# Kernel optimization log

Measured on AMD Instinct MI355X. Metric: run time of the kernel, lower is better.

Reference implementation:

```python
import jax, jax.numpy as jnp
import numpy as np

B, N = 16, 16384
K = 16        # num_keypoints
LATENT = 128
CAGE = 8
BN_EPS = 1e-5


def setup_inputs():
    key = jax.random.key(0)
    ks = jax.random.split(key, 40)
    def rn(i, shape, s=1.0):
        return jax.random.normal(ks[i], shape, dtype=jnp.float32) * s
    inp = {
        "source_points": rn(0, (B, N, 3)),
        "target_points": rn(1, (B, N, 3)),
        "enc_w1": rn(2, (64, 3), 0.3), "enc_b1": rn(3, (64,), 0.1),
        "bn1_gamma": 1.0 + rn(4, (64,), 0.1), "bn1_beta": rn(5, (64,), 0.1),
        "bn1_mean": rn(6, (64,), 0.1), "bn1_var": 0.5 + jax.random.uniform(ks[7], (64,), dtype=jnp.float32),
        "enc_w2": rn(8, (128, 64), 0.1), "enc_b2": rn(9, (128,), 0.1),
        "bn2_gamma": 1.0 + rn(10, (128,), 0.1), "bn2_beta": rn(11, (128,), 0.1),
        "bn2_mean": rn(12, (128,), 0.1), "bn2_var": 0.5 + jax.random.uniform(ks[13], (128,), dtype=jnp.float32),
        "enc_w3": rn(14, (LATENT, 128), 0.1), "enc_b3": rn(15, (LATENT,), 0.1),
        "bn3_gamma": 1.0 + rn(16, (LATENT,), 0.1), "bn3_beta": rn(17, (LATENT,), 0.1),
        "bn3_mean": rn(18, (LATENT,), 0.1), "bn3_var": 0.5 + jax.random.uniform(ks[19], (LATENT,), dtype=jnp.float32),
        "kp_w1": rn(20, (128, LATENT), 0.1), "kp_b1": rn(21, (128,), 0.1),
        "kp_w2": rn(22, (K * 3, 128), 0.1), "kp_b2": rn(23, (K * 3,), 0.1),
        "cg_w1": rn(24, (128, K * 3), 0.1), "cg_b1": rn(25, (128,), 0.1),
        "cg_w2": rn(26, (CAGE ** 3 * 3, 128), 0.05), "cg_b2": rn(27, (CAGE ** 3 * 3,), 0.01),
    }
    return inp


def _bn(x, g, b, m, v):
    # inference-mode BatchNorm1d over channel (last) dim
    return (x - m) * jax.lax.rsqrt(v + BN_EPS) * g + b


def _encode(pts, w1, b1, g1, be1, m1, v1, w2, b2, g2, be2, m2, v2, w3, b3, g3, be3, m3, v3):
    # pointwise 1x1 convs == per-point linear layers; pts: (B, N, 3)
    h = jax.nn.relu(_bn(jnp.einsum('bnc,oc->bno', pts, w1) + b1, g1, be1, m1, v1))
    h = jax.nn.relu(_bn(jnp.einsum('bnc,oc->bno', h, w2) + b2, g2, be2, m2, v2))
    h = jax.nn.relu(_bn(jnp.einsum('bnc,oc->bno', h, w3) + b3, g3, be3, m3, v3))
    return h.max(axis=1)  # global max-pool -> (B, LATENT)


def _fps_one(pts, kps):
    # pts: (N,3), kps: (K,3). Same math as the torch loop: iterative farthest-point
    # selection; recomputing cdist to selected[:i] each step == incremental min-dist.
    # squared distances preserve argmax/min of euclidean distances.
    d0 = jnp.sum((pts[:, None, :] - kps[None, :, :]) ** 2, -1).min(axis=1)
    sel0 = pts[jnp.argmax(d0)]
    mind = jnp.sum((pts - sel0) ** 2, -1)
    def step(mind, _):
        sel = pts[jnp.argmax(mind)]
        return jnp.minimum(mind, jnp.sum((pts - sel) ** 2, -1)), sel
    _, sels = jax.lax.scan(step, mind, None, length=K - 1)
    return jnp.concatenate([sel0[None], sels], axis=0)  # (K, 3)


def _fps(points, keypoints):
    return jax.vmap(_fps_one)(points, keypoints)


def _cage_deform(pts, disp):
    # pts: (B,N,3), disp: (B,C,C,C,3). Batched trilinear interpolation on the cage.
    C = CAGE
    lin = jnp.linspace(0.0, 1.0, C)
    grid = jnp.stack(jnp.meshgrid(lin, lin, lin, indexing='ij'), axis=-1)
    cage = grid[None] + disp
    cf = cage.reshape(cage.shape[0], C * C * C, 3)
    pmin = pts.min(axis=1, keepdims=True)
    pmax = pts.max(axis=1, keepdims=True)
    t = (pts - pmin) / (pmax - pmin + 1e-6) * (C - 1)
    idx = jnp.clip(t.astype(jnp.int32), 0, C - 2)   # trunc == floor (t >= 0)
    w = t - idx.astype(t.dtype)
    u, v, z = idx[..., 0], idx[..., 1], idx[..., 2]
    wx, wy, wz = w[..., 0:1], w[..., 1:2], w[..., 2:3]
    def corner(du, dv, dz):
        flat = (u + du) * C * C + (v + dv) * C + (z + dz)      # (B,N)
        flat = jnp.broadcast_to(flat[..., None], flat.shape + (3,))
        return jnp.take_along_axis(cf, flat, axis=1)            # (B,N,3)
    d = ((1 - wx) * (1 - wy) * (1 - wz) * corner(0, 0, 0)
         + wx * (1 - wy) * (1 - wz) * corner(1, 0, 0)
         + (1 - wx) * wy * (1 - wz) * corner(0, 1, 0)
         + wx * wy * (1 - wz) * corner(1, 1, 0)
         + (1 - wx) * (1 - wy) * wz * corner(0, 0, 1)
         + wx * (1 - wy) * wz * corner(1, 0, 1)
         + (1 - wx) * wy * wz * corner(0, 1, 1)
         + wx * wy * wz * corner(1, 1, 1))
    return pts + d


def reference(source_points, target_points, enc_w1, enc_b1, bn1_gamma, bn1_beta, bn1_mean, bn1_var, enc_w2, enc_b2, bn2_gamma, bn2_beta, bn2_mean, bn2_var, enc_w3, enc_b3, bn3_gamma, bn3_beta, bn3_mean, bn3_var, kp_w1, kp_b1, kp_w2, kp_b2, cg_w1, cg_b1, cg_w2, cg_b2):
    enc = lambda p: _encode(p, enc_w1, enc_b1, bn1_gamma, bn1_beta, bn1_mean, bn1_var,
                            enc_w2, enc_b2, bn2_gamma, bn2_beta, bn2_mean, bn2_var,
                            enc_w3, enc_b3, bn3_gamma, bn3_beta, bn3_mean, bn3_var)
    src_lat = enc(source_points)
    tgt_lat = enc(target_points)
    kp = lambda lat: (jax.nn.relu(lat @ kp_w1.T + kp_b1) @ kp_w2.T + kp_b2).reshape(-1, K, 3)
    src_kp = _fps(source_points, kp(src_lat))
    tgt_kp = _fps(target_points, kp(tgt_lat))
    diff = (tgt_kp - src_kp).reshape(-1, K * 3)
    disp = (jax.nn.relu(diff @ cg_w1.T + cg_b1) @ cg_w2.T + cg_b2).reshape(-1, CAGE, CAGE, CAGE, 3)
    deformed = _cage_deform(source_points, disp)
    return (deformed, src_kp, tgt_kp)
```

## Files before the change

### kernel.cpp

```cpp
#include <hip/hip_runtime.h>

#define B_ 16
#define N_ 16384
#define K_ 16

enum : int {
  WS_LAT  = 0,
  WS_SEL  = 5632,
  WS_PMIN = 7168,
  WS_PMAX = 7216,
  WS_CF   = 7264,
  WS_W1F  = 31840,
  WS_B1F  = 32032,
  WS_WB2H = 32096,
  WS_WB2L = 36192,
  WS_B2F  = 40288,
  WS_WB3H = 40416,
  WS_B3F  = 56800,
  WS_WB3L = 56928,
  WS_END  = 73312
};

enum : int { OUT_DEF=0, OUT_SRCKP=786432, OUT_TGTKP=787200 };

typedef _Float16 f16x8 __attribute__((ext_vector_type(8)));
typedef _Float16 f16x2 __attribute__((ext_vector_type(2)));
typedef float    f32x4 __attribute__((ext_vector_type(4)));

__device__ __forceinline__ float dist2rn(float px,float py,float pz,float sx,float sy,float sz){
  float dx=__fsub_rn(px,sx), dy=__fsub_rn(py,sy), dz=__fsub_rn(pz,sz);
  return __fadd_rn(__fadd_rn(__fmul_rn(dx,dx),__fmul_rn(dy,dy)),__fmul_rn(dz,dz));
}

struct EncW {
  const float *w1,*b1,*g1,*be1,*m1,*v1;
  const float *w2,*b2,*g2,*be2,*m2,*v2;
  const float *w3,*b3,*g3,*be3,*m3,*v3;
};

__device__ __forceinline__ float bn_scale(const float* g, const float* v, int ch){
  return g[ch] * (1.0f / sqrtf(v[ch] + 1e-5f));
}

__global__ void prep_kernel(EncW a, float* ws){
  const int stride = gridDim.x*blockDim.x;
  const int tid = blockIdx.x*blockDim.x + threadIdx.x;
  for (int i=tid;i<4096;i+=stride)
    ws[WS_LAT+i] = 0.0f;
  for (int i=tid;i<192;i+=stride){
    int o=i/3;
    ws[WS_W1F+i] = a.w1[i] * bn_scale(a.g1,a.v1,o);
  }
  for (int i=tid;i<64;i+=stride){
    float s = bn_scale(a.g1,a.v1,i);
    ws[WS_B1F+i] = (a.b1[i] - a.m1[i])*s + a.be1[i];
  }
  for (int i=tid;i<8192;i+=stride){
    int j = i & 7, frag = i >> 3;
    int l = frag & 63, nk = frag >> 6;
    int kt = nk & 1, nt = nk >> 1;
    int c = kt*32 + ((l>>4)<<3) + j;
    int o = nt*16 + (l&15);
    float v = a.w2[o*64+c] * bn_scale(a.g2,a.v2,o);
    _Float16 h = (_Float16)v;
    ((_Float16*)(ws+WS_WB2H))[i] = h;
    ((_Float16*)(ws+WS_WB2L))[i] = (_Float16)(v - (float)h);
  }
  for (int i=tid;i<128;i+=stride){
    float s = bn_scale(a.g2,a.v2,i);
    ws[WS_B2F+i] = (a.b2[i] - a.m2[i])*s + a.be2[i];
  }
  for (int i=tid;i<32768;i+=stride){
    int j = i & 7, frag = i >> 3;
    int l = frag & 63, nk = frag >> 6;
    int kt = nk & 3, nt = nk >> 2;
    int c = kt*32 + ((l>>4)<<3) + j;
    int o = nt*16 + (l&15);
    float v = a.w3[o*128+c] * bn_scale(a.g3,a.v3,o);
    _Float16 h = (_Float16)v;
    ((_Float16*)(ws+WS_WB3H))[i] = h;
    ((_Float16*)(ws+WS_WB3L))[i] = (_Float16)(v - (float)h);
  }
  for (int i=tid;i<128;i+=stride){
    float s = bn_scale(a.g3,a.v3,i);
    ws[WS_B3F+i] = (a.b3[i] - a.m3[i])*s + a.be3[i];
  }
}

__global__ __launch_bounds__(512, 4) void encode_kernel(const float* __restrict__ src,
                                                        const float* __restrict__ tgt,
                                                        const float* __restrict__ ws,
                                                        float* __restrict__ lat){
  const int cloud = blockIdx.y;
  const int tile  = blockIdx.x;
  const int t = threadIdx.x;
  const int lane = t & 63;
  const int wv = __builtin_amdgcn_readfirstlane(t >> 6);
  const int wm = wv >> 2;
  const int wn = wv & 3;
  const int lr = lane & 15;
  const int lg = lane >> 4;

  __shared__ alignas(16) _Float16 A[32768];
  _Float16* AH1 = A;
  _Float16* AL1 = A + 8192;
  _Float16* AH2 = A;
  _Float16* AL2 = A + 16384;

  const float* base = ((cloud < B_) ? (src + (size_t)cloud*N_*3)
                                    : (tgt + (size_t)(cloud-B_)*N_*3))
                      + (size_t)tile*128*3;

  {
    const int pt = t >> 2, q = t & 3;
    const float x = base[pt*3+0], y = base[pt*3+1], z = base[pt*3+2];
    const float* w1 = ws + WS_W1F;
    const float* b1 = ws + WS_B1F;
    const int swz = (pt & 7) << 3;
    #pragma unroll
    for (int cc = 0; cc < 16; cc += 2){
      const int o = q*16 + cc;
      float v0 = fmaf(w1[o*3+2], z, fmaf(w1[o*3+1], y, w1[o*3+0]*x)) + b1[o];
      float v1 = fmaf(w1[o*3+5], z, fmaf(w1[o*3+4], y, w1[o*3+3]*x)) + b1[o+1];
      v0 = fmaxf(v0, 0.0f); v1 = fmaxf(v1, 0.0f);
      f16x2 h, l;
      h[0] = (_Float16)v0;              h[1] = (_Float16)v1;
      l[0] = (_Float16)(v0 - (float)h[0]); l[1] = (_Float16)(v1 - (float)h[1]);
      const int idx = (pt*64 + o) ^ swz;
      *(f16x2*)&AH1[idx] = h;
      *(f16x2*)&AL1[idx] = l;
    }
  }
  __syncthreads();

  f32x4 acc2[4][2];
  #pragma unroll
  for (int m=0;m<4;m++){
    #pragma unroll
    for (int n=0;n<2;n++) acc2[m][n] = (f32x4){0.f,0.f,0.f,0.f};
  }
  {
    const _Float16* wb2h = (const _Float16*)(ws + WS_WB2H);
    const _Float16* wb2l = (const _Float16*)(ws + WS_WB2L);
    const int swz = (lr & 7) << 3;
    #pragma unroll
    for (int kt=0; kt<2; kt++){
      f16x8 bh[2], bl[2];
      #pragma unroll
      for (int n=0;n<2;n++){
        const int fi = (((wn*2+n)*2 + kt)*64 + lane)*8;
        bh[n] = *(const f16x8*)(wb2h + fi);
        bl[n] = *(const f16x8*)(wb2l + fi);
      }
      #pragma unroll
      for (int m=0;m<4;m++){
        const int row = wm*64 + m*16 + lr;
        const int idx = (row*64 + kt*32 + lg*8) ^ swz;
        const f16x8 ah = *(const f16x8*)&AH1[idx];
        const f16x8 al = *(const f16x8*)&AL1[idx];
        #pragma unroll
        for (int n=0;n<2;n++){
          acc2[m][n] = __builtin_amdgcn_mfma_f32_16x16x32_f16(ah, bh[n], acc2[m][n], 0,0,0);
          acc2[m][n] = __builtin_amdgcn_mfma_f32_16x16x32_f16(ah, bl[n], acc2[m][n], 0,0,0);
          acc2[m][n] = __builtin_amdgcn_mfma_f32_16x16x32_f16(al, bh[n], acc2[m][n], 0,0,0);
        }
      }
    }
  }
  __syncthreads();

  {
    const float* b2 = ws + WS_B2F;
    #pragma unroll
    for (int n=0;n<2;n++){
      const int ch = wn*32 + n*16 + lr;
      const float b = b2[ch];
      #pragma unroll
      for (int m=0;m<4;m++){
        #pragma unroll
        for (int r=0;r<4;r++){
          const int row = wm*64 + m*16 + lg*4 + r;
          const float v = fmaxf(acc2[m][n][r] + b, 0.0f);
          const _Float16 hi = (_Float16)v;
          const _Float16 lo = (_Float16)(v - (float)hi);
          const int idx = (row*128 + ch) ^ ((row & 7) << 3);
          AH2[idx] = hi;
          AL2[idx] = lo;
        }
      }
    }
  }
  __syncthreads();

  f32x4 acc3[4][2];
  #pragma unroll
  for (int m=0;m<4;m++){
    #pragma unroll
    for (int n=0;n<2;n++) acc3[m][n] = (f32x4){0.f,0.f,0.f,0.f};
  }
  {
    const _Float16* wb3h = (const _Float16*)(ws + WS_WB3H);
    const _Float16* wb3l = (const _Float16*)(ws + WS_WB3L);
    const int swz = (lr & 7) << 3;
    #pragma unroll
    for (int kt=0; kt<4; kt++){
      f16x8 bh[2], bl[2];
      #pragma unroll
      for (int n=0;n<2;n++){
        const int fi = (((wn*2+n)*4 + kt)*64 + lane)*8;
        bh[n] = *(const f16x8*)(wb3h + fi);
        bl[n] = *(const f16x8*)(wb3l + fi);
      }
      #pragma unroll
      for (int m=0;m<4;m++){
        const int row = wm*64 + m*16 + lr;
        const int idx = (row*128 + kt*32 + lg*8) ^ swz;
        const f16x8 ah = *(const f16x8*)&AH2[idx];
        const f16x8 al = *(const f16x8*)&AL2[idx];
        #pragma unroll
        for (int n=0;n<2;n++){
          acc3[m][n] = __builtin_amdgcn_mfma_f32_16x16x32_f16(ah, bh[n], acc3[m][n], 0,0,0);
          acc3[m][n] = __builtin_amdgcn_mfma_f32_16x16x32_f16(ah, bl[n], acc3[m][n], 0,0,0);
          acc3[m][n] = __builtin_amdgcn_mfma_f32_16x16x32_f16(al, bh[n], acc3[m][n], 0,0,0);
        }
      }
    }
  }

  {
    const float* b3 = ws + WS_B3F;
    #pragma unroll
    for (int n=0;n<2;n++){
      const int ch = wn*32 + n*16 + lr;
      const float b = b3[ch];
      float x = 0.0f;
      #pragma unroll
      for (int m=0;m<4;m++){
        #pragma unroll
        for (int r=0;r<4;r++)
          x = fmaxf(x, acc3[m][n][r] + b);
      }
      x = fmaxf(x, __shfl_xor(x, 16, 64));
      x = fmaxf(x, __shfl_xor(x, 32, 64));
      if (lane < 16)
        atomicMax((unsigned*)(lat + cloud*128 + ch), __float_as_uint(x));
    }
  }
}

__global__ __launch_bounds__(512) void fps_kernel(const float* __restrict__ src,
                                                  const float* __restrict__ tgt,
                                                  const float* __restrict__ kw1,
                                                  const float* __restrict__ kb1,
                                                  const float* __restrict__ kw2,
                                                  const float* __restrict__ kb2,
                                                  float* ws, float* out){
  const int cloud = blockIdx.x; const int t = threadIdx.x;
  const float* base = (cloud < B_) ? (src + (size_t)cloud*N_*3)
                                   : (tgt + (size_t)(cloud-B_)*N_*3);
  __shared__ float kpl[48];
  __shared__ float h[128];
  __shared__ float rv[512]; __shared__ int ri[512];
  __shared__ float sel[3];

  float px[32], py[32], pz[32];
  #pragma unroll
  for (int k=0;k<32;k++){
    int n = t + k*512;
    px[k]=base[n*3]; py[k]=base[n*3+1]; pz[k]=base[n*3+2];
  }

  const float* lat = ws + WS_LAT + cloud*128;
  if (t < 128){
    float acc = kb1[t];
    const float* w = kw1 + t*128;
    for (int c=0;c<128;c++) acc = fmaf(lat[c], w[c], acc);
    h[t] = fmaxf(acc, 0.0f);
  }
  __syncthreads();
  if (t < 48){
    float acc = kb2[t];
    const float* w = kw2 + t*128;
    for (int c=0;c<128;c++) acc = fmaf(h[c], w[c], acc);
    kpl[t] = acc;
  }
  __syncthreads();

  float mnx=3.4e38f,mny=3.4e38f,mnz=3.4e38f, mxx=-3.4e38f,mxy=-3.4e38f,mxz=-3.4e38f;
  float bv = -1.0f; int bi = 0;
  #pragma unroll 2
  for (int k=0;k<32;k++){
    int n = t + k*512;
    if (cloud < B_){
      mnx=fminf(mnx,px[k]); mny=fminf(mny,py[k]); mnz=fminf(mnz,pz[k]);
      mxx=fmaxf(mxx,px[k]); mxy=fmaxf(mxy,py[k]); mxz=fmaxf(mxz,pz[k]);
    }
    float dmin = 3.4028235e38f;
    #pragma unroll
    for (int j=0;j<K_;j++)
      dmin = fminf(dmin, dist2rn(px[k],py[k],pz[k], kpl[j*3],kpl[j*3+1],kpl[j*3+2]));
    if (dmin > bv){ bv = dmin; bi = n; }
  }

  rv[t]=bv; ri[t]=bi;
  __syncthreads();
  if (t < 64){
    float v = rv[t]; int i = ri[t];
    #pragma unroll
    for (int e=1;e<8;e++){
      float v2=rv[t+64*e]; int i2=ri[t+64*e];
      if (v2 > v || (v2 == v && i2 < i)){ v=v2; i=i2; }
    }
    #pragma unroll
    for (int m=1;m<64;m<<=1){
      float v2=__shfl_xor(v,m,64); int i2=__shfl_xor(i,m,64);
      if (v2 > v || (v2 == v && i2 < i)){ v=v2; i=i2; }
    }
    if (t==0){
      sel[0]=base[i*3]; sel[1]=base[i*3+1]; sel[2]=base[i*3+2];
      float* sw = ws + WS_SEL + cloud*48;
      sw[0]=sel[0]; sw[1]=sel[1]; sw[2]=sel[2];
      size_t o = (cloud<B_) ? (size_t)(OUT_SRCKP + cloud*48) : (size_t)(OUT_TGTKP + (cloud-B_)*48);
      out[o]=sel[0]; out[o+1]=sel[1]; out[o+2]=sel[2];
    }
  }
  __syncthreads();

  if (cloud < B_){
    float vals[6] = {mnx,mny,mnz,mxx,mxy,mxz};
    for (int c=0;c<6;c++){
      rv[t]=vals[c];
      __syncthreads();
      if (t < 64){
        float v = rv[t];
        #pragma unroll
        for (int e=1;e<8;e++){
          float v2 = rv[t+64*e];
          v = (c<3) ? fminf(v,v2) : fmaxf(v,v2);
        }
        #pragma unroll
        for (int m=1;m<64;m<<=1){
          float v2=__shfl_xor(v,m,64);
          v = (c<3) ? fminf(v,v2) : fmaxf(v,v2);
        }
        if (t==0){
          if (c<3) ws[WS_PMIN + cloud*3 + c] = v;
          else     ws[WS_PMAX + cloud*3 + (c-3)] = v;
        }
      }
      __syncthreads();
    }
  }

  float s0=sel[0], s1=sel[1], s2=sel[2];

  float mind[32];
  bv = -1.0f; bi = 0;
  #pragma unroll
  for (int k=0;k<32;k++){
    int n = t + k*512;
    float d = dist2rn(px[k],py[k],pz[k], s0,s1,s2);
    mind[k]=d;
    if (d > bv){ bv=d; bi=n; }
  }

  for (int it=1; it<K_; it++){
    rv[t]=bv; ri[t]=bi;
    __syncthreads();
    if (t < 64){
      float v = rv[t]; int i = ri[t];
      #pragma unroll
      for (int e=1;e<8;e++){
        float v2=rv[t+64*e]; int i2=ri[t+64*e];
        if (v2 > v || (v2 == v && i2 < i)){ v=v2; i=i2; }
      }
      #pragma unroll
      for (int m=1;m<64;m<<=1){
        float v2=__shfl_xor(v,m,64); int i2=__shfl_xor(i,m,64);
        if (v2 > v || (v2 == v && i2 < i)){ v=v2; i=i2; }
      }
      if (t==0){
        sel[0]=base[i*3]; sel[1]=base[i*3+1]; sel[2]=base[i*3+2];
        float* sw = ws + WS_SEL + cloud*48 + it*3;
        sw[0]=sel[0]; sw[1]=sel[1]; sw[2]=sel[2];
        size_t o = (cloud<B_) ? (size_t)(OUT_SRCKP + cloud*48 + it*3)
                              : (size_t)(OUT_TGTKP + (cloud-B_)*48 + it*3);
        out[o]=sel[0]; out[o+1]=sel[1]; out[o+2]=sel[2];
      }
    }
    __syncthreads();
    s0=sel[0]; s1=sel[1]; s2=sel[2];
    if (it < K_-1){
      bv=-1.0f; bi=0;
      #pragma unroll
      for (int k=0;k<32;k++){
        int n = t + k*512;
        float d = dist2rn(px[k],py[k],pz[k], s0,s1,s2);
        float m = fminf(mind[k], d);
        mind[k]=m;
        if (m > bv){ bv=m; bi=n; }
      }
    }
  }
}

__global__ void cage_mlp_kernel(const float* __restrict__ ws,
                                const float* __restrict__ cw1, const float* __restrict__ cb1,
                                const float* __restrict__ cw2, const float* __restrict__ cb2,
                                float* __restrict__ wsm){
  const int b = blockIdx.x >> 2, part = blockIdx.x & 3;
  const int t = threadIdx.x;
  __shared__ float diff[48]; __shared__ float h[128];
  if (t<48) diff[t] = __fsub_rn(ws[WS_SEL + (B_+b)*48 + t], ws[WS_SEL + b*48 + t]);
  __syncthreads();
  if (t<128){
    const float* w = cw1 + t*48;
    float acc = cb1[t];
    for (int j=0;j<48;j++) acc = fmaf(diff[j], w[j], acc);
    h[t] = fmaxf(acc, 0.0f);
  }
  __syncthreads();
  for (int o = part*384 + t; o < part*384 + 384; o += 256){
    const float* w = cw2 + o*128;
    float acc = cb2[o];
    for (int c=0;c<128;c++) acc = fmaf(h[c], w[c], acc);
    int flat = o/3, coord = o - flat*3;
    int u = flat>>6, v=(flat>>3)&7, z=flat&7;
    int g = (coord==0)?u:((coord==1)?v:z);
    float gv = (g==7)?1.0f:(float)g*(1.0f/7.0f);
    wsm[WS_CF + b*1536 + o] = gv + acc;
  }
}

__global__ __launch_bounds__(256) void deform_kernel(const float* __restrict__ src,
                                                     const float* __restrict__ ws,
                                                     float* __restrict__ out){
  const int b = blockIdx.y;
  const int n = blockIdx.x*256 + threadIdx.x;
  __shared__ float cf[1536];
  for (int i=threadIdx.x;i<1536;i+=256) cf[i] = ws[WS_CF + b*1536 + i];
  __syncthreads();

  const float* p = src + ((size_t)b*N_ + n)*3;
  float pt[3]; int id[3]; float w[3];
  #pragma unroll
  for (int c=0;c<3;c++){
    float pv = p[c];
    float mn = ws[WS_PMIN+b*3+c], mxv = ws[WS_PMAX+b*3+c];
    float denom = __fadd_rn(__fsub_rn(mxv, mn), 1e-6f);
    float tc = __fmul_rn(__fdiv_rn(__fsub_rn(pv, mn), denom), 7.0f);
    int ic = (int)tc; ic = min(max(ic,0),6);
    pt[c]=pv; id[c]=ic; w[c]=__fsub_rn(tc, (float)ic);
  }
  const int flat = (id[0]<<6) + (id[1]<<3) + id[2];
  const float* c000 = cf + flat*3;
  const float wx=w[0], wy=w[1], wz=w[2];
  const float ux=__fsub_rn(1.0f,wx), uy=__fsub_rn(1.0f,wy), uz=__fsub_rn(1.0f,wz);
  const float w000=__fmul_rn(__fmul_rn(ux,uy),uz);
  const float w100=__fmul_rn(__fmul_rn(wx,uy),uz);
  const float w010=__fmul_rn(__fmul_rn(ux,wy),uz);
  const float w110=__fmul_rn(__fmul_rn(wx,wy),uz);
  const float w001=__fmul_rn(__fmul_rn(ux,uy),wz);
  const float w101=__fmul_rn(__fmul_rn(wx,uy),wz);
  const float w011=__fmul_rn(__fmul_rn(ux,wy),wz);
  const float w111=__fmul_rn(__fmul_rn(wx,wy),wz);
  #pragma unroll
  for (int c=0;c<3;c++){
    float d = __fmul_rn(w000, c000[c]);
    d = __fadd_rn(d, __fmul_rn(w100, c000[192+c]));
    d = __fadd_rn(d, __fmul_rn(w010, c000[24+c]));
    d = __fadd_rn(d, __fmul_rn(w110, c000[216+c]));
    d = __fadd_rn(d, __fmul_rn(w001, c000[3+c]));
    d = __fadd_rn(d, __fmul_rn(w101, c000[195+c]));
    d = __fadd_rn(d, __fmul_rn(w011, c000[27+c]));
    d = __fadd_rn(d, __fmul_rn(w111, c000[219+c]));
    out[((size_t)b*N_+n)*3 + c] = __fadd_rn(pt[c], d);
  }
}

extern "C" void kernel_launch(void* const* d_in, const int* in_sizes, int n_in,
                              void* d_out, int out_size, void* d_ws, size_t ws_size,
                              hipStream_t stream){
  const float* src = (const float*)d_in[0];
  const float* tgt = (const float*)d_in[1];
  float* ws = (float*)d_ws;
  float* out = (float*)d_out;

  EncW ew;
  ew.w1 =(const float*)d_in[2];  ew.b1 =(const float*)d_in[3];
  ew.g1 =(const float*)d_in[4];  ew.be1=(const float*)d_in[5];
  ew.m1 =(const float*)d_in[6];  ew.v1 =(const float*)d_in[7];
  ew.w2 =(const float*)d_in[8];  ew.b2 =(const float*)d_in[9];
  ew.g2 =(const float*)d_in[10]; ew.be2=(const float*)d_in[11];
  ew.m2 =(const float*)d_in[12]; ew.v2 =(const float*)d_in[13];
  ew.w3 =(const float*)d_in[14]; ew.b3 =(const float*)d_in[15];
  ew.g3 =(const float*)d_in[16]; ew.be3=(const float*)d_in[17];
  ew.m3 =(const float*)d_in[18]; ew.v3 =(const float*)d_in[19];

  prep_kernel<<<128, 256, 0, stream>>>(ew, ws);
  encode_kernel<<<dim3(128,32), 512, 0, stream>>>(src, tgt, ws, ws + WS_LAT);
  fps_kernel<<<32, 512, 0, stream>>>(src, tgt,
      (const float*)d_in[20], (const float*)d_in[21],
      (const float*)d_in[22], (const float*)d_in[23], ws, out);
  cage_mlp_kernel<<<64, 256, 0, stream>>>(ws,
      (const float*)d_in[24], (const float*)d_in[25],
      (const float*)d_in[26], (const float*)d_in[27], ws);
  deform_kernel<<<dim3(64,16), 256, 0, stream>>>(src, ws, out);
}
```

Before: 302.6 us.

## Restructure FPS kernel with 1024 threads, single-barrier rounds, and separate minmax kernel

Moves the per-cloud bounding-box min/max out of the FPS kernel into a new minmax_kernel that writes order-preserving encoded floats through atomics. The FPS kernel now runs 1024 threads per cloud, and each thread loads 16 contiguous points with float4 reads. Each round does a wave-level shuffle argmax and carries the winner's coordinates, so a single barrier and double-buffered shared slots replace the two-barrier shared reduction and the global reload of the selected point. The intent is to cut per-iteration latency in the serial 16-round FPS loop, at the cost of an extra kernel launch and atomic traffic.

```diff
diff --git a/kernel.cpp b/kernel.cpp
--- a/kernel.cpp
+++ b/kernel.cpp
@@ -32,6 +32,14 @@
   return __fadd_rn(__fadd_rn(__fmul_rn(dx,dx),__fmul_rn(dy,dy)),__fmul_rn(dz,dz));
 }
 
+__device__ __forceinline__ unsigned enc_ord(float x){
+  unsigned u = __float_as_uint(x);
+  return (u & 0x80000000u) ? ~u : (u | 0x80000000u);
+}
+__device__ __forceinline__ float dec_ord(unsigned e){
+  return __uint_as_float((e & 0x80000000u) ? (e & 0x7fffffffu) : ~e);
+}
+
 struct EncW {
   const float *w1,*b1,*g1,*be1,*m1,*v1;
   const float *w2,*b2,*g2,*be2,*m2,*v2;
@@ -47,6 +55,10 @@
   const int tid = blockIdx.x*blockDim.x + threadIdx.x;
   for (int i=tid;i<4096;i+=stride)
     ws[WS_LAT+i] = 0.0f;
+  for (int i=tid;i<48;i+=stride){
+    ((unsigned*)ws)[WS_PMIN+i] = 0xFFFFFFFFu;
+    ((unsigned*)ws)[WS_PMAX+i] = 0u;
+  }
   for (int i=tid;i<192;i+=stride){
     int o=i/3;
     ws[WS_W1F+i] = a.w1[i] * bn_scale(a.g1,a.v1,o);
@@ -84,6 +96,38 @@
   for (int i=tid;i<128;i+=stride){
     float s = bn_scale(a.g3,a.v3,i);
     ws[WS_B3F+i] = (a.b3[i] - a.m3[i])*s + a.be3[i];
+  }
+}
+
+__global__ __launch_bounds__(256) void minmax_kernel(const float* __restrict__ src,
+                                                     float* __restrict__ ws){
+  const int b = blockIdx.y, c = blockIdx.x, t = threadIdx.x;
+  const float4* b4 = (const float4*)(src + (size_t)b*N_*3 + (size_t)c*2048*3 + (size_t)t*24);
+  float a[24];
+  #pragma unroll
+  for (int q=0;q<6;q++){ float4 v=b4[q]; a[q*4]=v.x; a[q*4+1]=v.y; a[q*4+2]=v.z; a[q*4+3]=v.w; }
+  float mn[3]={3.4e38f,3.4e38f,3.4e38f}, mx[3]={-3.4e38f,-3.4e38f,-3.4e38f};
+  #pragma unroll
+  for (int k=0;k<8;k++){
+    mn[0]=fminf(mn[0],a[k*3  ]); mx[0]=fmaxf(mx[0],a[k*3  ]);
+    mn[1]=fminf(mn[1],a[k*3+1]); mx[1]=fmaxf(mx[1],a[k*3+1]);
+    mn[2]=fminf(mn[2],a[k*3+2]); mx[2]=fmaxf(mx[2],a[k*3+2]);
+  }
+  #pragma unroll
+  for (int m=1;m<64;m<<=1){
+    #pragma unroll
+    for (int cc=0;cc<3;cc++){
+      mn[cc]=fminf(mn[cc],__shfl_xor(mn[cc],m,64));
+      mx[cc]=fmaxf(mx[cc],__shfl_xor(mx[cc],m,64));
+    }
+  }
+  if ((t&63)==0){
+    unsigned* wsu = (unsigned*)ws;
+    #pragma unroll
+    for (int cc=0;cc<3;cc++){
+      atomicMin(&wsu[WS_PMIN + b*3 + cc], enc_ord(mn[cc]));
+      atomicMax(&wsu[WS_PMAX + b*3 + cc], enc_ord(mx[cc]));
+    }
   }
 }
 
@@ -248,26 +292,61 @@
   }
 }
 
-__global__ __launch_bounds__(512) void fps_kernel(const float* __restrict__ src,
-                                                  const float* __restrict__ tgt,
-                                                  const float* __restrict__ kw1,
-                                                  const float* __restrict__ kb1,
-                                                  const float* __restrict__ kw2,
-                                                  const float* __restrict__ kb2,
-                                                  float* ws, float* out){
+__device__ __forceinline__ void fps_round(int r, int t, int wv,
+                                          float bv, int bi, float bx, float by, float bz,
+                                          float (*cv)[16], int (*ci)[16],
+                                          float (*cx)[16], float (*cy)[16], float (*cz)[16],
+                                          float* ws, float* out, int cloud,
+                                          float& s0, float& s1, float& s2){
+  float v = bv; int i = bi;
+  #pragma unroll
+  for (int m=1;m<64;m<<=1){
+    float v2=__shfl_xor(v,m,64); int i2=__shfl_xor(i,m,64);
+    if (v2 > v || (v2 == v && i2 < i)){ v=v2; i=i2; }
+  }
+  const int p = r & 1;
+  if ((i >> 4) == t){ cv[p][wv]=v; ci[p][wv]=i; cx[p][wv]=bx; cy[p][wv]=by; cz[p][wv]=bz; }
+  __syncthreads();
+  float wvv = cv[p][0]; int wi = ci[p][0]; int ws_slot = 0;
+  #pragma unroll
+  for (int e=1;e<16;e++){
+    float v2=cv[p][e]; int i2=ci[p][e];
+    if (v2 > wvv || (v2 == wvv && i2 < wi)){ wvv=v2; wi=i2; ws_slot=e; }
+  }
+  s0 = cx[p][ws_slot]; s1 = cy[p][ws_slot]; s2 = cz[p][ws_slot];
+  if (t == 0){
+    float* sw = ws + WS_SEL + cloud*48 + r*3;
+    sw[0]=s0; sw[1]=s1; sw[2]=s2;
+    size_t o = (cloud<B_) ? (size_t)(OUT_SRCKP + cloud*48 + r*3)
+                          : (size_t)(OUT_TGTKP + (cloud-B_)*48 + r*3);
+    out[o]=s0; out[o+1]=s1; out[o+2]=s2;
+  }
+}
+
+__global__ __launch_bounds__(1024) void fps_kernel(const float* __restrict__ src,
+                                                   const float* __restrict__ tgt,
+                                                   const float* __restrict__ kw1,
+                                                   const float* __restrict__ kb1,
+                                                   const float* __restrict__ kw2,
+                                                   const float* __restrict__ kb2,
+                                                   float* ws, float* out){
   const int cloud = blockIdx.x; const int t = threadIdx.x;
+  const int wv = t >> 6;
   const float* base = (cloud < B_) ? (src + (size_t)cloud*N_*3)
                                    : (tgt + (size_t)(cloud-B_)*N_*3);
   __shared__ float kpl[48];
   __shared__ float h[128];
-  __shared__ float rv[512]; __shared__ int ri[512];
-  __shared__ float sel[3];
-
-  float px[32], py[32], pz[32];
-  #pragma unroll
-  for (int k=0;k<32;k++){
-    int n = t + k*512;
-    px[k]=base[n*3]; py[k]=base[n*3+1]; pz[k]=base[n*3+2];
+  __shared__ float cv[2][16]; __shared__ int ci[2][16];
+  __shared__ float cx[2][16]; __shared__ float cy[2][16]; __shared__ float cz[2][16];
+
+  float px[16], py[16], pz[16];
+  {
+    const float4* b4 = (const float4*)(base + (size_t)t*48);
+    float a[48];
+    #pragma unroll
+    for (int q=0;q<12;q++){ float4 v=b4[q]; a[q*4]=v.x; a[q*4+1]=v.y; a[q*4+2]=v.z; a[q*4+3]=v.w; }
+    #pragma unroll
+    for (int k=0;k<16;k++){ px[k]=a[k*3]; py[k]=a[k*3+1]; pz[k]=a[k*3+2]; }
   }
 
   const float* lat = ws + WS_LAT + cloud*128;
@@ -286,121 +365,43 @@
   }
   __syncthreads();
 
-  float mnx=3.4e38f,mny=3.4e38f,mnz=3.4e38f, mxx=-3.4e38f,mxy=-3.4e38f,mxz=-3.4e38f;
-  float bv = -1.0f; int bi = 0;
-  #pragma unroll 2
-  for (int k=0;k<32;k++){
-    int n = t + k*512;
-    if (cloud < B_){
-      mnx=fminf(mnx,px[k]); mny=fminf(mny,py[k]); mnz=fminf(mnz,pz[k]);
-      mxx=fmaxf(mxx,px[k]); mxy=fmaxf(mxy,py[k]); mxz=fmaxf(mxz,pz[k]);
-    }
-    float dmin = 3.4028235e38f;
-    #pragma unroll
-    for (int j=0;j<K_;j++)
-      dmin = fminf(dmin, dist2rn(px[k],py[k],pz[k], kpl[j*3],kpl[j*3+1],kpl[j*3+2]));
-    if (dmin > bv){ bv = dmin; bi = n; }
-  }
-
-  rv[t]=bv; ri[t]=bi;
-  __syncthreads();
-  if (t < 64){
-    float v = rv[t]; int i = ri[t];
-    #pragma unroll
-    for (int e=1;e<8;e++){
-      float v2=rv[t+64*e]; int i2=ri[t+64*e];
-      if (v2 > v || (v2 == v && i2 < i)){ v=v2; i=i2; }
-    }
-    #pragma unroll
-    for (int m=1;m<64;m<<=1){
-      float v2=__shfl_xor(v,m,64); int i2=__shfl_xor(i,m,64);
-      if (v2 > v || (v2 == v && i2 < i)){ v=v2; i=i2; }
-    }
-    if (t==0){
-      sel[0]=base[i*3]; sel[1]=base[i*3+1]; sel[2]=base[i*3+2];
-      float* sw = ws + WS_SEL + cloud*48;
-      sw[0]=sel[0]; sw[1]=sel[1]; sw[2]=sel[2];
-      size_t o = (cloud<B_) ? (size_t)(OUT_SRCKP + cloud*48) : (size_t)(OUT_TGTKP + (cloud-B_)*48);
-      out[o]=sel[0]; out[o+1]=sel[1]; out[o+2]=sel[2];
-    }
-  }
-  __syncthreads();
-
-  if (cloud < B_){
-    float vals[6] = {mnx,mny,mnz,mxx,mxy,mxz};
-    for (int c=0;c<6;c++){
-      rv[t]=vals[c];
-      __syncthreads();
-      if (t < 64){
-        float v = rv[t];
-        #pragma unroll
-        for (int e=1;e<8;e++){
-          float v2 = rv[t+64*e];
-          v = (c<3) ? fminf(v,v2) : fmaxf(v,v2);
-        }
-        #pragma unroll
-        for (int m=1;m<64;m<<=1){
-          float v2=__shfl_xor(v,m,64);
-          v = (c<3) ? fminf(v,v2) : fmaxf(v,v2);
-        }
-        if (t==0){
-          if (c<3) ws[WS_PMIN + cloud*3 + c] = v;
-          else     ws[WS_PMAX + cloud*3 + (c-3)] = v;
-        }
-      }
-      __syncthreads();
-    }
-  }
-
-  float s0=sel[0], s1=sel[1], s2=sel[2];
-
-  float mind[32];
+  float mind[16];
+  #pragma unroll
+  for (int k=0;k<16;k++) mind[k] = 3.4028235e38f;
+  for (int j=0;j<K_;j++){
+    const float sx=kpl[j*3], sy=kpl[j*3+1], sz=kpl[j*3+2];
+    #pragma unroll
+    for (int k=0;k<16;k++)
+      mind[k] = fminf(mind[k], dist2rn(px[k],py[k],pz[k], sx,sy,sz));
+  }
+
+  float bv = -1.0f; int bi = 0; float bx=0.f, by=0.f, bz=0.f;
+  #pragma unroll
+  for (int k=0;k<16;k++){
+    if (mind[k] > bv){ bv=mind[k]; bi=t*16+k; bx=px[k]; by=py[k]; bz=pz[k]; }
+  }
+  float s0, s1, s2;
+  fps_round(0, t, wv, bv, bi, bx, by, bz, cv, ci, cx, cy, cz, ws, out, cloud, s0, s1, s2);
+
   bv = -1.0f; bi = 0;
   #pragma unroll
-  for (int k=0;k<32;k++){
-    int n = t + k*512;
+  for (int k=0;k<16;k++){
     float d = dist2rn(px[k],py[k],pz[k], s0,s1,s2);
-    mind[k]=d;
-    if (d > bv){ bv=d; bi=n; }
-  }
-
-  for (int it=1; it<K_; it++){
-    rv[t]=bv; ri[t]=bi;
-    __syncthreads();
-    if (t < 64){
-      float v = rv[t]; int i = ri[t];
-      #pragma unroll
-      for (int e=1;e<8;e++){
-        float v2=rv[t+64*e]; int i2=ri[t+64*e];
-        if (v2 > v || (v2 == v && i2 < i)){ v=v2; i=i2; }
-      }
-      #pragma unroll
-      for (int m=1;m<64;m<<=1){
-        float v2=__shfl_xor(v,m,64); int i2=__shfl_xor(i,m,64);
-        if (v2 > v || (v2 == v && i2 < i)){ v=v2; i=i2; }
-      }
-      if (t==0){
-        sel[0]=base[i*3]; sel[1]=base[i*3+1]; sel[2]=base[i*3+2];
-        float* sw = ws + WS_SEL + cloud*48 + it*3;
-        sw[0]=sel[0]; sw[1]=sel[1]; sw[2]=sel[2];
-        size_t o = (cloud<B_) ? (size_t)(OUT_SRCKP + cloud*48 + it*3)
-                              : (size_t)(OUT_TGTKP + (cloud-B_)*48 + it*3);
-        out[o]=sel[0]; out[o+1]=sel[1]; out[o+2]=sel[2];
-      }
-    }
-    __syncthreads();
-    s0=sel[0]; s1=sel[1]; s2=sel[2];
-    if (it < K_-1){
-      bv=-1.0f; bi=0;
-      #pragma unroll
-      for (int k=0;k<32;k++){
-        int n = t + k*512;
-        float d = dist2rn(px[k],py[k],pz[k], s0,s1,s2);
-        float m = fminf(mind[k], d);
-        mind[k]=m;
-        if (m > bv){ bv=m; bi=n; }
-      }
-    }
+    mind[k] = d;
+    if (d > bv){ bv=d; bi=t*16+k; bx=px[k]; by=py[k]; bz=pz[k]; }
+  }
+  fps_round(1, t, wv, bv, bi, bx, by, bz, cv, ci, cx, cy, cz, ws, out, cloud, s0, s1, s2);
+
+  for (int r=2; r<K_; ++r){
+    bv = -1.0f; bi = 0;
+    #pragma unroll
+    for (int k=0;k<16;k++){
+      float d = dist2rn(px[k],py[k],pz[k], s0,s1,s2);
+      float m = fminf(mind[k], d);
+      mind[k] = m;
+      if (m > bv){ bv=m; bi=t*16+k; bx=px[k]; by=py[k]; bz=pz[k]; }
+    }
+    fps_round(r, t, wv, bv, bi, bx, by, bz, cv, ci, cx, cy, cz, ws, out, cloud, s0, s1, s2);
   }
 }
 
@@ -446,7 +447,8 @@
   #pragma unroll
   for (int c=0;c<3;c++){
     float pv = p[c];
-    float mn = ws[WS_PMIN+b*3+c], mxv = ws[WS_PMAX+b*3+c];
+    float mn  = dec_ord(((const unsigned*)ws)[WS_PMIN+b*3+c]);
+    float mxv = dec_ord(((const unsigned*)ws)[WS_PMAX+b*3+c]);
     float denom = __fadd_rn(__fsub_rn(mxv, mn), 1e-6f);
     float tc = __fmul_rn(__fdiv_rn(__fsub_rn(pv, mn), denom), 7.0f);
     int ic = (int)tc; ic = min(max(ic,0),6);
@@ -498,8 +500,9 @@
   ew.m3 =(const float*)d_in[18]; ew.v3 =(const float*)d_in[19];
 
   prep_kernel<<<128, 256, 0, stream>>>(ew, ws);
+  minmax_kernel<<<dim3(8,16), 256, 0, stream>>>(src, ws);
   encode_kernel<<<dim3(128,32), 512, 0, stream>>>(src, tgt, ws, ws + WS_LAT);
-  fps_kernel<<<32, 512, 0, stream>>>(src, tgt,
+  fps_kernel<<<32, 1024, 0, stream>>>(src, tgt,
       (const float*)d_in[20], (const float*)d_in[21],
       (const float*)d_in[22], (const float*)d_in[23], ws, out);
   cage_mlp_kernel<<<64, 256, 0, stream>>>(ws,
```

Result: slower. 320.2 us (+5.8%).
